# Performance work log

Measured on AMD Instinct MI355X. Metric: run time of the kernel, lower is better.

Reference implementation:

```python
import jax, jax.numpy as jnp
import numpy as np

ALPHA = 0.95
BETA = 0.9

def setup_inputs() -> dict:
    key = jax.random.key(0)
    k1, k2 = jax.random.split(key)
    B, T, I, O = 64, 1000, 512, 256
    inputs = jax.random.normal(k1, (B, T, I), dtype=jnp.float32)
    W = jax.random.normal(k2, (O, I), dtype=jnp.float32) * (1.0 / np.sqrt(I))
    return {"inputs": inputs, "W": W, "nb_steps": T}

def reference(inputs, W, nb_steps):
    B = inputs.shape[0]
    O = W.shape[0]
    # linear projection: h[b,t,o]
    h = jnp.einsum('bti,oi->bto', inputs, W)
    h_t = jnp.swapaxes(h, 0, 1)  # (T, B, O) for scan over time

    def step(carry, ht):
        flt, out = carry
        new_flt = ALPHA * flt + ht
        new_out = BETA * out + flt  # uses OLD flt, matching the torch loop
        return (new_flt, new_out), new_out

    init = (jnp.zeros((B, O), jnp.float32), jnp.zeros((B, O), jnp.float32))
    _, out_rec = jax.lax.scan(step, init, h_t)
    return jnp.swapaxes(out_rec, 0, 1)  # (B, T, O)
```

## Files before the change

### kernel.cpp

```cpp
#include <hip/hip_runtime.h>
#include <hip/hip_bf16.h>
#include <stdint.h>


#define ALPHA 0.95f
#define BETA  0.9f

constexpr int Bdim = 64, T = 1000, Idim = 512, Odim = 256;
constexpr int M = Bdim * T;
constexpr int C = 40, L = 25;

typedef short bf16x8 __attribute__((ext_vector_type(8)));
typedef float f32x4  __attribute__((ext_vector_type(4)));

__device__ inline uint32_t pk_bf16(float a, float b) {
  union { float f; uint32_t u; } x, y; x.f = a; y.f = b;
  uint32_t lo = (x.u + 0x7FFFu + ((x.u >> 16) & 1u)) >> 16;
  uint32_t hi = (y.u + 0x7FFFu + ((y.u >> 16) & 1u)) & 0xFFFF0000u;
  return lo | hi;
}
__device__ inline uint16_t f2bf(float a) {
  union { float f; uint32_t u; } x; x.f = a;
  return (uint16_t)((x.u + 0x7FFFu + ((x.u >> 16) & 1u)) >> 16);
}
__device__ inline float bf2f(uint16_t h) {
  union { uint32_t u; float f; } x; x.u = ((uint32_t)h) << 16;
  return x.f;
}

#define GLD16(g, l) __builtin_amdgcn_global_load_lds(                         \
    (const __attribute__((address_space(1))) uint32_t*)(g),                   \
    (__attribute__((address_space(3))) uint32_t*)(l), 16, 0, 0)

__device__ inline bf16x8 cvt8(float4 x0, float4 x1) {
  union { __hip_bfloat162 h[4]; bf16x8 v; } r;
  r.h[0] = __float22bfloat162_rn(make_float2(x0.x, x0.y));
  r.h[1] = __float22bfloat162_rn(make_float2(x0.z, x0.w));
  r.h[2] = __float22bfloat162_rn(make_float2(x1.x, x1.y));
  r.h[3] = __float22bfloat162_rn(make_float2(x1.z, x1.w));
  return r.v;
}

__global__ __launch_bounds__(256) void wconv(const float* __restrict__ W,
                                             uint16_t* __restrict__ Wbf) {
  int i = (blockIdx.x * 256 + threadIdx.x) * 8;
  float4 a = *(const float4*)(W + i);
  float4 b = *(const float4*)(W + i + 4);
  *(uint4*)(Wbf + i) = make_uint4(pk_bf16(a.x, a.y), pk_bf16(a.z, a.w),
                                  pk_bf16(b.x, b.y), pk_bf16(b.z, b.w));
}

__global__ __launch_bounds__(256) void gemm_h(const float* __restrict__ A,
                                              const uint16_t* __restrict__ Wbf,
                                              uint16_t* __restrict__ H) {
  __shared__ float    As[64 * 32];
  __shared__ uint16_t Bs[256 * 32];

  const int tid  = threadIdx.x;
  const int lane = tid & 63;
  const int w    = tid >> 6;
  const int l15  = lane & 15;
  const int quad = lane >> 4;
  const int rm   = blockIdx.x * 64;

  const int ar = w * 8 + (lane >> 3);
  const int akc = (lane & 7) ^ ((lane >> 3) & 7);
  const int br = w * 16 + (lane >> 2);
  const int bkc = (lane & 3) ^ ((lane >> 2) & 3);

  const float*    ag0 = A   + (size_t)(rm + ar) * Idim + akc * 4;
  const float*    ag1 = A   + (size_t)(rm + 32 + ar) * Idim + akc * 4;
  const uint16_t* bg[4];
#pragma unroll
  for (int p = 0; p < 4; ++p) bg[p] = Wbf + (size_t)(p * 64 + br) * Idim + bkc * 8;

  char* al0 = (char*)As + w * 1024;
  char* al1 = (char*)As + 4096 + w * 1024;
  char* bl[4];
#pragma unroll
  for (int p = 0; p < 4; ++p) bl[p] = (char*)Bs + p * 4096 + w * 1024;

  int aoff0[4], aoff1[4], boff[4];
#pragma unroll
  for (int t = 0; t < 4; ++t) {
    int m = t * 16 + l15;
    aoff0[t] = m * 32 + (((2 * quad)     ^ (m & 7)) * 4);
    aoff1[t] = m * 32 + (((2 * quad + 1) ^ (m & 7)) * 4);
    int n = w * 64 + t * 16 + l15;
    boff[t] = n * 32 + ((quad ^ (n & 3)) * 8);
  }

  f32x4 acc[4][4] = {};

  for (int k0 = 0; k0 < Idim; k0 += 32) {
    __syncthreads();
    GLD16(ag0 + k0, al0);
    GLD16(ag1 + k0, al1);
#pragma unroll
    for (int p = 0; p < 4; ++p) GLD16(bg[p] + k0, bl[p]);
    __syncthreads();

    bf16x8 af[4], bfr[4];
#pragma unroll
    for (int t = 0; t < 4; ++t) {
      float4 x0 = *(const float4*)&As[aoff0[t]];
      float4 x1 = *(const float4*)&As[aoff1[t]];
      af[t] = cvt8(x0, x1);
    }
#pragma unroll
    for (int t = 0; t < 4; ++t) bfr[t] = *(const bf16x8*)&Bs[boff[t]];
#pragma unroll
    for (int mt = 0; mt < 4; ++mt)
#pragma unroll
      for (int nt = 0; nt < 4; ++nt)
        acc[mt][nt] = __builtin_amdgcn_mfma_f32_16x16x32_bf16(af[mt], bfr[nt], acc[mt][nt], 0, 0, 0);
  }

#pragma unroll
  for (int mt = 0; mt < 4; ++mt)
#pragma unroll
    for (int nt = 0; nt < 4; ++nt)
#pragma unroll
      for (int r = 0; r < 4; ++r) {
        int gm = rm + mt * 16 + quad * 4 + r;
        int gn = w * 64 + nt * 16 + l15;
        H[(size_t)gm * Odim + gn] = f2bf(acc[mt][nt][r]);
      }
}

constexpr double dpow(double x, int n) { double r = 1.0; for (int i = 0; i < n; ++i) r *= x; return r; }

__global__ __launch_bounds__(640) void scan_all(const uint16_t* __restrict__ H,
                                                float* __restrict__ Out) {
  constexpr float AL = (float)dpow(0.95, L);
  constexpr float BL = (float)dpow(0.90, L);
  constexpr float WL = (float)((dpow(0.95, L) - dpow(0.90, L)) / (0.95 - 0.90));
  __shared__ float2 St[C][64];

  const int b  = blockIdx.x >> 2;
  const int og = blockIdx.x & 3;
  const int tid = threadIdx.x;
  const int c  = tid >> 4;
  const int ol = tid & 15;

  const size_t base = ((size_t)b * T + c * L) * Odim + og * 64 + ol * 4;
  const ushort4* hp = (const ushort4*)(H + base);

  {
    float f[4] = {}, u[4] = {};
#pragma unroll
    for (int j = 0; j < L; ++j) {
      ushort4 hv = hp[j * 64];
      float h0 = bf2f(hv.x), h1 = bf2f(hv.y), h2 = bf2f(hv.z), h3 = bf2f(hv.w);
      float n0 = BETA * u[0] + f[0]; f[0] = ALPHA * f[0] + h0; u[0] = n0;
      float n1 = BETA * u[1] + f[1]; f[1] = ALPHA * f[1] + h1; u[1] = n1;
      float n2 = BETA * u[2] + f[2]; f[2] = ALPHA * f[2] + h2; u[2] = n2;
      float n3 = BETA * u[3] + f[3]; f[3] = ALPHA * f[3] + h3; u[3] = n3;
    }
#pragma unroll
    for (int i = 0; i < 4; ++i) St[c][ol * 4 + i] = make_float2(f[i], u[i]);
  }
  __syncthreads();

  if (tid < 64) {
    float f = 0.f, u = 0.f;
#pragma unroll
    for (int cc = 0; cc < C; ++cc) {
      float2 s = St[cc][tid];
      St[cc][tid] = make_float2(f, u);
      float nu = BL * u + WL * f + s.y;
      f = AL * f + s.x;
      u = nu;
    }
  }
  __syncthreads();

  {
    float f[4], u[4];
#pragma unroll
    for (int i = 0; i < 4; ++i) { float2 s = St[c][ol * 4 + i]; f[i] = s.x; u[i] = s.y; }
    float4* op = (float4*)(Out + base);
#pragma unroll
    for (int j = 0; j < L; ++j) {
      ushort4 hv = hp[j * 64];
      float h0 = bf2f(hv.x), h1 = bf2f(hv.y), h2 = bf2f(hv.z), h3 = bf2f(hv.w);
      float4 o4;
      o4.x = BETA * u[0] + f[0]; f[0] = ALPHA * f[0] + h0; u[0] = o4.x;
      o4.y = BETA * u[1] + f[1]; f[1] = ALPHA * f[1] + h1; u[1] = o4.y;
      o4.z = BETA * u[2] + f[2]; f[2] = ALPHA * f[2] + h2; u[2] = o4.z;
      o4.w = BETA * u[3] + f[3]; f[3] = ALPHA * f[3] + h3; u[3] = o4.w;
      op[j * 64] = o4;
    }
  }
}

extern "C" void kernel_launch(void* const* d_in, const int* in_sizes, int n_in,
                              void* d_out, int out_size, void* d_ws, size_t ws_size,
                              hipStream_t stream) {
  const float* A = (const float*)d_in[0];
  const float* W = (const float*)d_in[1];
  float* Out = (float*)d_out;

  uint16_t* H   = (uint16_t*)d_ws;
  uint16_t* Wbf = H + (size_t)M * Odim;

  wconv<<<Odim * Idim / (256 * 8), 256, 0, stream>>>(W, Wbf);
  gemm_h<<<M / 64, 256, 0, stream>>>(A, Wbf, H);
  scan_all<<<Bdim * 4, 640, 0, stream>>>(H, Out);
}
```

Measured before the change: 247.2 us.

## Load GEMM operands directly from global into registers; cache H in scan registers

The GEMM drops the LDS staging and per-k-step barriers. Each lane now loads its own A and W fragments straight from global memory, with register double-buffering of the next A slice and launch bounds that target 3 blocks per CU. The scan kernel keeps the 25 loaded H values per thread in registers, so the second pass no longer re-reads H from global. The trade-offs are more uncoalesced, redundant global loads in the GEMM, since each wave re-reads W and A without LDS sharing, and higher register pressure in both kernels.

```diff
diff --git a/kernel.cpp b/kernel.cpp
--- a/kernel.cpp
+++ b/kernel.cpp
@@ -28,10 +28,6 @@
   return x.f;
 }
 
-#define GLD16(g, l) __builtin_amdgcn_global_load_lds(                         \
-    (const __attribute__((address_space(1))) uint32_t*)(g),                   \
-    (__attribute__((address_space(3))) uint32_t*)(l), 16, 0, 0)
-
 __device__ inline bf16x8 cvt8(float4 x0, float4 x1) {
   union { __hip_bfloat162 h[4]; bf16x8 v; } r;
   r.h[0] = __float22bfloat162_rn(make_float2(x0.x, x0.y));
@@ -50,12 +46,9 @@
                                   pk_bf16(b.x, b.y), pk_bf16(b.z, b.w));
 }
 
-__global__ __launch_bounds__(256) void gemm_h(const float* __restrict__ A,
-                                              const uint16_t* __restrict__ Wbf,
-                                              uint16_t* __restrict__ H) {
-  __shared__ float    As[64 * 32];
-  __shared__ uint16_t Bs[256 * 32];
-
+__global__ __launch_bounds__(256, 3) void gemm_h(const float* __restrict__ A,
+                                                 const uint16_t* __restrict__ Wbf,
+                                                 uint16_t* __restrict__ H) {
   const int tid  = threadIdx.x;
   const int lane = tid & 63;
   const int w    = tid >> 6;
@@ -63,57 +56,53 @@
   const int quad = lane >> 4;
   const int rm   = blockIdx.x * 64;
 
-  const int ar = w * 8 + (lane >> 3);
-  const int akc = (lane & 7) ^ ((lane >> 3) & 7);
-  const int br = w * 16 + (lane >> 2);
-  const int bkc = (lane & 3) ^ ((lane >> 2) & 3);
-
-  const float*    ag0 = A   + (size_t)(rm + ar) * Idim + akc * 4;
-  const float*    ag1 = A   + (size_t)(rm + 32 + ar) * Idim + akc * 4;
-  const uint16_t* bg[4];
-#pragma unroll
-  for (int p = 0; p < 4; ++p) bg[p] = Wbf + (size_t)(p * 64 + br) * Idim + bkc * 8;
-
-  char* al0 = (char*)As + w * 1024;
-  char* al1 = (char*)As + 4096 + w * 1024;
-  char* bl[4];
-#pragma unroll
-  for (int p = 0; p < 4; ++p) bl[p] = (char*)Bs + p * 4096 + w * 1024;
-
-  int aoff0[4], aoff1[4], boff[4];
+  const float*    ap[4];
+  const uint16_t* bp[4];
 #pragma unroll
   for (int t = 0; t < 4; ++t) {
-    int m = t * 16 + l15;
-    aoff0[t] = m * 32 + (((2 * quad)     ^ (m & 7)) * 4);
-    aoff1[t] = m * 32 + (((2 * quad + 1) ^ (m & 7)) * 4);
-    int n = w * 64 + t * 16 + l15;
-    boff[t] = n * 32 + ((quad ^ (n & 3)) * 8);
+    ap[t] = A   + (size_t)(rm + t * 16 + l15) * Idim + quad * 8;
+    bp[t] = Wbf + (size_t)(w * 64 + t * 16 + l15) * Idim + quad * 8;
   }
 
   f32x4 acc[4][4] = {};
 
-  for (int k0 = 0; k0 < Idim; k0 += 32) {
-    __syncthreads();
-    GLD16(ag0 + k0, al0);
-    GLD16(ag1 + k0, al1);
+  float4 ca[4][2];
 #pragma unroll
-    for (int p = 0; p < 4; ++p) GLD16(bg[p] + k0, bl[p]);
-    __syncthreads();
+  for (int t = 0; t < 4; ++t) {
+    ca[t][0] = *(const float4*)(ap[t]);
+    ca[t][1] = *(const float4*)(ap[t] + 4);
+  }
 
-    bf16x8 af[4], bfr[4];
+#pragma unroll
+  for (int ks = 0; ks < 16; ++ks) {
+    bf16x8 bfr[4];
 #pragma unroll
     for (int t = 0; t < 4; ++t) {
-      float4 x0 = *(const float4*)&As[aoff0[t]];
-      float4 x1 = *(const float4*)&As[aoff1[t]];
-      af[t] = cvt8(x0, x1);
+      union { uint4 u; bf16x8 v; } bb;
+      bb.u = *(const uint4*)(bp[t] + ks * 32);
+      bfr[t] = bb.v;
     }
+    float4 na[4][2];
+    if (ks < 15) {
+      const int ko = (ks + 1) * 32;
 #pragma unroll
-    for (int t = 0; t < 4; ++t) bfr[t] = *(const bf16x8*)&Bs[boff[t]];
+      for (int t = 0; t < 4; ++t) {
+        na[t][0] = *(const float4*)(ap[t] + ko);
+        na[t][1] = *(const float4*)(ap[t] + ko + 4);
+      }
+    }
+    bf16x8 af[4];
+#pragma unroll
+    for (int t = 0; t < 4; ++t) af[t] = cvt8(ca[t][0], ca[t][1]);
 #pragma unroll
     for (int mt = 0; mt < 4; ++mt)
 #pragma unroll
       for (int nt = 0; nt < 4; ++nt)
         acc[mt][nt] = __builtin_amdgcn_mfma_f32_16x16x32_bf16(af[mt], bfr[nt], acc[mt][nt], 0, 0, 0);
+    if (ks < 15) {
+#pragma unroll
+      for (int t = 0; t < 4; ++t) { ca[t][0] = na[t][0]; ca[t][1] = na[t][1]; }
+    }
   }
 
 #pragma unroll
@@ -137,21 +126,22 @@
   constexpr float WL = (float)((dpow(0.95, L) - dpow(0.90, L)) / (0.95 - 0.90));
   __shared__ float2 St[C][64];
 
-  const int b  = blockIdx.x >> 2;
-  const int og = blockIdx.x & 3;
+  const int b   = blockIdx.x >> 2;
+  const int og  = blockIdx.x & 3;
   const int tid = threadIdx.x;
-  const int c  = tid >> 4;
-  const int ol = tid & 15;
+  const int c   = tid >> 4;
+  const int ol  = tid & 15;
 
   const size_t base = ((size_t)b * T + c * L) * Odim + og * 64 + ol * 4;
   const ushort4* hp = (const ushort4*)(H + base);
 
+  ushort4 hv[L];
   {
     float f[4] = {}, u[4] = {};
 #pragma unroll
     for (int j = 0; j < L; ++j) {
-      ushort4 hv = hp[j * 64];
-      float h0 = bf2f(hv.x), h1 = bf2f(hv.y), h2 = bf2f(hv.z), h3 = bf2f(hv.w);
+      hv[j] = hp[j * 64];
+      float h0 = bf2f(hv[j].x), h1 = bf2f(hv[j].y), h2 = bf2f(hv[j].z), h3 = bf2f(hv[j].w);
       float n0 = BETA * u[0] + f[0]; f[0] = ALPHA * f[0] + h0; u[0] = n0;
       float n1 = BETA * u[1] + f[1]; f[1] = ALPHA * f[1] + h1; u[1] = n1;
       float n2 = BETA * u[2] + f[2]; f[2] = ALPHA * f[2] + h2; u[2] = n2;
@@ -182,8 +172,7 @@
     float4* op = (float4*)(Out + base);
 #pragma unroll
     for (int j = 0; j < L; ++j) {
-      ushort4 hv = hp[j * 64];
-      float h0 = bf2f(hv.x), h1 = bf2f(hv.y), h2 = bf2f(hv.z), h3 = bf2f(hv.w);
+      float h0 = bf2f(hv[j].x), h1 = bf2f(hv[j].y), h2 = bf2f(hv[j].z), h3 = bf2f(hv[j].w);
       float4 o4;
       o4.x = BETA * u[0] + f[0]; f[0] = ALPHA * f[0] + h0; u[0] = o4.x;
       o4.y = BETA * u[1] + f[1]; f[1] = ALPHA * f[1] + h1; u[1] = o4.y;
```

After: 273.2 us. +10.5%, slower.
